# Kernel tuning notes

Measured on AMD Instinct MI355X. Metric: run time of the kernel, lower is better.

Reference implementation:

```python
import jax, jax.numpy as jnp
import numpy as np

HEADS = 8
DIM_HEAD = 64
SCALE = DIM_HEAD ** -0.5
EPS = 1e-5


def layernorm(t, g, b):
    mu = t.mean(-1, keepdims=True)
    var = ((t - mu) ** 2).mean(-1, keepdims=True)
    return (t - mu) * jax.lax.rsqrt(var + EPS) * g + b


def setup_inputs() -> dict:
    key = jax.random.key(0)
    ks = jax.random.split(key, 12)
    b, n, dim, inner = 2, 2048, 512, HEADS * DIM_HEAD
    s = dim ** -0.5
    return {
        "x": jax.random.normal(ks[0], (b, n, dim), jnp.float32),
        "context": jax.random.normal(ks[1], (b, n, dim), jnp.float32),
        "g_x": jnp.ones((dim,), jnp.float32),
        "b_x": jnp.zeros((dim,), jnp.float32),
        "g_c": jnp.ones((dim,), jnp.float32),
        "b_c": jnp.zeros((dim,), jnp.float32),
        "W_qk": jax.random.normal(ks[2], (dim, inner), jnp.float32) * s,
        "W_cqk": jax.random.normal(ks[3], (dim, inner), jnp.float32) * s,
        "W_v": jax.random.normal(ks[4], (dim, inner), jnp.float32) * s,
        "W_cv": jax.random.normal(ks[5], (dim, inner), jnp.float32) * s,
        "W_out": jax.random.normal(ks[6], (inner, dim), jnp.float32) * s,
        "b_out": jnp.zeros((dim,), jnp.float32),
        "W_cout": jax.random.normal(ks[7], (inner, dim), jnp.float32) * s,
        "b_cout": jnp.zeros((dim,), jnp.float32),
    }


def reference(x, context, g_x, b_x, g_c, b_c, W_qk, W_cqk, W_v, W_cv, W_out, b_out, W_cout, b_cout):
    b, i, _ = x.shape
    j = context.shape[1]
    xn = layernorm(x, g_x, b_x)
    cn = layernorm(context, g_c, b_c)

    def split_heads(t):  # [b, n, h*d] -> [b, h, n, d]
        return t.reshape(t.shape[0], t.shape[1], HEADS, DIM_HEAD).transpose(0, 2, 1, 3)

    qk = split_heads(xn @ W_qk)
    cqk = split_heads(cn @ W_cqk)
    v = split_heads(xn @ W_v)
    cv = split_heads(cn @ W_cv)

    sim = jnp.einsum('bhid,bhjd->bhij', qk, cqk) * SCALE  # [b,h,i,j]
    attn = jax.nn.softmax(sim, axis=-1)           # rows: x attends to context
    context_attn = jax.nn.softmax(sim, axis=-2)   # cols: context attends to x

    out = jnp.einsum('bhij,bhjd->bhid', attn, cv)            # [b,h,i,d]
    context_out = jnp.einsum('bhij,bhid->bhjd', context_attn, v)  # [b,h,j,d]

    def merge_heads(t):  # [b,h,n,d] -> [b,n,h*d]
        return t.transpose(0, 2, 1, 3).reshape(t.shape[0], t.shape[2], HEADS * DIM_HEAD)

    out = merge_heads(out) @ W_out + b_out
    context_out = merge_heads(context_out) @ W_cout + b_cout
    return out, context_out
```

## Files before the change

kernel.cpp:

```cpp
#include <hip/hip_runtime.h>


typedef _Float16 half_t;
typedef __attribute__((ext_vector_type(4))) _Float16 half4v;
typedef __attribute__((ext_vector_type(8))) _Float16 half8v;
typedef __attribute__((ext_vector_type(4))) float floatx4;

#define MFMA16(a, b, c) __builtin_amdgcn_mfma_f32_16x16x32_f16((a), (b), (c), 0, 0, 0)

#if defined(__has_builtin)
#if __has_builtin(__builtin_amdgcn_exp2f)
#define EXP2F(x) __builtin_amdgcn_exp2f(x)
#else
#define EXP2F(x) exp2f(x)
#endif
#else
#define EXP2F(x) exp2f(x)
#endif

__device__ __forceinline__ void gld16(const half_t* g, half_t* l) {
    __builtin_amdgcn_global_load_lds(
        (const __attribute__((address_space(1))) void*)g,
        (__attribute__((address_space(3))) void*)l, 16, 0, 0);
}

__global__ __launch_bounds__(256) void prep_kernel(
    const float* __restrict__ x, const float* __restrict__ ctx,
    const float* __restrict__ gx, const float* __restrict__ bx,
    const float* __restrict__ gc, const float* __restrict__ bc,
    half_t* __restrict__ xn, half_t* __restrict__ cn,
    const float* __restrict__ W0, const float* __restrict__ W1,
    const float* __restrict__ W2, const float* __restrict__ W3,
    const float* __restrict__ W4, const float* __restrict__ W5,
    half_t* __restrict__ Wt)
{
    __shared__ alignas(16) half_t Ts[128][136];
    const int blk = blockIdx.x;
    const int tid = threadIdx.x;
    const int wave = tid >> 6, lane = tid & 63;

    if (blk < 2048) {
        const int row = blk * 4 + wave;
        const float *src, *g, *b;
        half_t* dst;
        if (row < 4096) {
            src = x + (size_t)row * 512; g = gx; b = bx; dst = xn + (size_t)row * 512;
        } else {
            const size_t r = (size_t)(row - 4096);
            src = ctx + r * 512; g = gc; b = bc; dst = cn + r * 512;
        }
        const float4 a0 = *(const float4*)(src + lane * 4);
        const float4 a1 = *(const float4*)(src + 256 + lane * 4);
        float s = a0.x + a0.y + a0.z + a0.w + a1.x + a1.y + a1.z + a1.w;
        float q = a0.x * a0.x + a0.y * a0.y + a0.z * a0.z + a0.w * a0.w +
                  a1.x * a1.x + a1.y * a1.y + a1.z * a1.z + a1.w * a1.w;
#pragma unroll
        for (int m = 1; m < 64; m <<= 1) {
            s += __shfl_xor(s, m);
            q += __shfl_xor(q, m);
        }
        const float mean = s * (1.0f / 512.0f);
        const float var = q * (1.0f / 512.0f) - mean * mean;
        const float rs = rsqrtf(var + 1e-5f);
        const float4 g0 = *(const float4*)(g + lane * 4);
        const float4 g1 = *(const float4*)(g + 256 + lane * 4);
        const float4 b0 = *(const float4*)(b + lane * 4);
        const float4 b1 = *(const float4*)(b + 256 + lane * 4);
        half4v h0, h1;
        h0[0] = (half_t)((a0.x - mean) * rs * g0.x + b0.x);
        h0[1] = (half_t)((a0.y - mean) * rs * g0.y + b0.y);
        h0[2] = (half_t)((a0.z - mean) * rs * g0.z + b0.z);
        h0[3] = (half_t)((a0.w - mean) * rs * g0.w + b0.w);
        h1[0] = (half_t)((a1.x - mean) * rs * g1.x + b1.x);
        h1[1] = (half_t)((a1.y - mean) * rs * g1.y + b1.y);
        h1[2] = (half_t)((a1.z - mean) * rs * g1.z + b1.z);
        h1[3] = (half_t)((a1.w - mean) * rs * g1.w + b1.w);
        *(half4v*)(dst + lane * 4) = h0;
        *(half4v*)(dst + 256 + lane * 4) = h1;
        return;
    }

    const int b2 = blk - 2048;
    const int mat = b2 >> 4, tile = b2 & 15;
    const float* src;
    switch (mat) {
        case 0: src = W0; break;
        case 1: src = W1; break;
        case 2: src = W2; break;
        case 3: src = W3; break;
        case 4: src = W4; break;
        default: src = W5; break;
    }
    const int tr0 = (tile >> 2) * 128;
    const int tc0 = (tile & 3) * 128;
#pragma unroll
    for (int p = 0; p < 16; ++p) {
        const int idx = p * 256 + tid;
        const int r = idx >> 5, c4 = (idx & 31) * 4;
        const float4 w = *(const float4*)(src + (size_t)(tr0 + r) * 512 + tc0 + c4);
        Ts[c4 + 0][r] = (half_t)w.x;
        Ts[c4 + 1][r] = (half_t)w.y;
        Ts[c4 + 2][r] = (half_t)w.z;
        Ts[c4 + 3][r] = (half_t)w.w;
    }
    __syncthreads();
    half_t* dst = Wt + (size_t)mat * 262144;
#pragma unroll
    for (int p = 0; p < 8; ++p) {
        const int idx = p * 256 + tid;
        const int row = idx >> 4, ch = (idx & 15) * 8;
        *(half8v*)(dst + (size_t)(tc0 + row) * 512 + tr0 + ch) = *(const half8v*)&Ts[row][ch];
    }
}

__global__ __launch_bounds__(256) void gemm_in_kernel(
    const half_t* __restrict__ xn, const half_t* __restrict__ cn,
    const half_t* __restrict__ Wt,
    half_t* __restrict__ qk, half_t* __restrict__ v_t,
    half_t* __restrict__ cqk, half_t* __restrict__ cv_t)
{
    const half_t* A; const half_t* B; half_t* O;
    switch (blockIdx.z) {
        case 0:  A = xn; B = Wt;          O = qk;   break;
        case 1:  A = xn; B = Wt + 262144; O = v_t;  break;
        case 2:  A = cn; B = Wt + 524288; O = cqk;  break;
        default: A = cn; B = Wt + 786432; O = cv_t; break;
    }
    const int tr = blockIdx.z & 1;
    const int mt0 = blockIdx.x * 128;
    const int nt0 = blockIdx.y * 128;

    __shared__ alignas(16) half_t As[128 * 64];
    __shared__ alignas(16) half_t Ws[128 * 64];

    const int tid = threadIdx.x;
    const int wave = tid >> 6, lane = tid & 63;
    const int wr = wave >> 1, wc = wave & 1;
    const int q4 = lane >> 4, c = lane & 15;

    int srow[4], scol[4];
#pragma unroll
    for (int p = 0; p < 4; ++p) {
        const int ofs = p * 4096 + wave * 1024 + lane * 16;
        const int row = ofs >> 7;
        const int pc = (ofs >> 4) & 7;
        srow[p] = row;
        scol[p] = (pc ^ (row & 7)) * 8;
    }

    const half_t* P1 = tr ? As : Ws;
    const half_t* P2 = tr ? Ws : As;

    const floatx4 z4 = {0.f, 0.f, 0.f, 0.f};
    floatx4 acc[4][4];
#pragma unroll
    for (int mt = 0; mt < 4; ++mt)
#pragma unroll
        for (int nt = 0; nt < 4; ++nt) acc[mt][nt] = z4;

    for (int kb = 0; kb < 8; ++kb) {
        const int k0 = kb * 64;
#pragma unroll
        for (int p = 0; p < 4; ++p) {
            const int lofs = p * 2048 + wave * 512;
            gld16(A + (size_t)(mt0 + srow[p]) * 512 + k0 + scol[p], As + lofs);
            gld16(B + (size_t)(nt0 + srow[p]) * 512 + k0 + scol[p], Ws + lofs);
        }
        __syncthreads();
#pragma unroll
        for (int kt = 0; kt < 2; ++kt) {
            half8v f1[4], f2[4];
#pragma unroll
            for (int i = 0; i < 4; ++i) {
                const int r1 = wr * 64 + i * 16 + c;
                const int r2 = wc * 64 + i * 16 + c;
                f1[i] = *(const half8v*)&P1[(r1 << 6) + (((kt * 4 + q4) ^ (r1 & 7)) << 3)];
                f2[i] = *(const half8v*)&P2[(r2 << 6) + (((kt * 4 + q4) ^ (r2 & 7)) << 3)];
            }
#pragma unroll
            for (int mt = 0; mt < 4; ++mt)
#pragma unroll
                for (int nt = 0; nt < 4; ++nt)
                    acc[mt][nt] = MFMA16(f1[mt], f2[nt], acc[mt][nt]);
        }
        __syncthreads();
    }

    const int bb = mt0 >> 11;
    const int nnb = mt0 & 2047;
    if (tr) {
#pragma unroll
        for (int mt = 0; mt < 4; ++mt) {
            const int row = nnb + wr * 64 + mt * 16 + q4 * 4;
#pragma unroll
            for (int nt = 0; nt < 4; ++nt) {
                const int col = nt0 + wc * 64 + nt * 16 + c;
                const int h = col >> 6, dd = col & 63;
                half4v pk;
                pk[0] = (half_t)acc[mt][nt][0];
                pk[1] = (half_t)acc[mt][nt][1];
                pk[2] = (half_t)acc[mt][nt][2];
                pk[3] = (half_t)acc[mt][nt][3];
                *(half4v*)(O + ((size_t)(bb * 8 + h) * 64 + dd) * 2048 + row) = pk;
            }
        }
    } else {
#pragma unroll
        for (int mt = 0; mt < 4; ++mt) {
            const int colw = nt0 + wr * 64 + mt * 16 + q4 * 4;
            const int h = colw >> 6, dd = colw & 63;
#pragma unroll
            for (int nt = 0; nt < 4; ++nt) {
                const int row = nnb + wc * 64 + nt * 16 + c;
                half4v pk;
                pk[0] = (half_t)acc[mt][nt][0];
                pk[1] = (half_t)acc[mt][nt][1];
                pk[2] = (half_t)acc[mt][nt][2];
                pk[3] = (half_t)acc[mt][nt][3];
                *(half4v*)(O + ((size_t)(bb * 8 + h) * 2048 + row) * 64 + dd) = pk;
            }
        }
    }
}

__global__ __launch_bounds__(256, 2) void flash_kernel(
    const half_t* __restrict__ qk, const half_t* __restrict__ cqk,
    const half_t* __restrict__ v_t, const half_t* __restrict__ cv_t,
    half_t* __restrict__ out_h, half_t* __restrict__ ctx_out_h)
{
    const int it = blockIdx.x, bh = blockIdx.y, dir = blockIdx.z;
    const half_t* Q  = dir ? cqk : qk;
    const half_t* K  = dir ? qk  : cqk;
    const half_t* VT = dir ? v_t : cv_t;
    half_t* Out = dir ? ctx_out_h : out_h;
    const half_t* Qb = Q + (size_t)bh * (2048 * 64);
    const half_t* Kb = K + (size_t)bh * (2048 * 64);
    const half_t* VTb = VT + (size_t)bh * (64 * 2048);

    __shared__ alignas(16) half_t Ks[128][72];
    __shared__ alignas(16) half_t CVs[64][136];
    __shared__ alignas(16) half_t Ps[128][72];

    const int tid = threadIdx.x;
    const int wave = tid >> 6, lane = tid & 63;
    const int q4 = lane >> 4, c = lane & 15;

    half8v onesb;
#pragma unroll
    for (int j = 0; j < 8; ++j) onesb[j] = (c == 0) ? (half_t)1.0f : (half_t)0.0f;

    half8v qf[2][2];
#pragma unroll
    for (int mt = 0; mt < 2; ++mt)
#pragma unroll
        for (int kt = 0; kt < 2; ++kt) {
            half8v v = *(const half8v*)(Qb + (size_t)(it * 128 + wave * 32 + mt * 16 + c) * 64 +
                                        kt * 32 + q4 * 8);
            qf[mt][kt] = v * (half_t)0.18033688f;
        }

    const floatx4 z4 = {0.f, 0.f, 0.f, 0.f};
    floatx4 accT[4][2];
    floatx4 accL[2];
#pragma unroll
    for (int vt = 0; vt < 4; ++vt)
#pragma unroll
        for (int mt = 0; mt < 2; ++mt) accT[vt][mt] = z4;
    accL[0] = z4; accL[1] = z4;

    half8v kpre[4], vpre[4];
#pragma unroll
    for (int p = 0; p < 4; ++p) {
        const int cidx = p * 256 + tid;
        kpre[p] = *(const half8v*)(Kb + (size_t)(cidx >> 3) * 64 + (cidx & 7) * 8);
        vpre[p] = *(const half8v*)(VTb + (size_t)(cidx >> 4) * 2048 + (cidx & 15) * 8);
    }

    for (int jt = 0; jt < 16; ++jt) {
        __syncthreads();
#pragma unroll
        for (int p = 0; p < 4; ++p) {
            const int cidx = p * 256 + tid;
            *(half8v*)&Ks[cidx >> 3][(cidx & 7) * 8] = kpre[p];
            *(half8v*)&CVs[cidx >> 4][(cidx & 15) * 8] = vpre[p];
        }
        __syncthreads();
        if (jt < 15) {
            const half_t* Kt = Kb + (size_t)(jt + 1) * 8192;
            const half_t* Vt = VTb + (jt + 1) * 128;
#pragma unroll
            for (int p = 0; p < 4; ++p) {
                const int cidx = p * 256 + tid;
                kpre[p] = *(const half8v*)(Kt + (size_t)(cidx >> 3) * 64 + (cidx & 7) * 8);
                vpre[p] = *(const half8v*)(Vt + (size_t)(cidx >> 4) * 2048 + (cidx & 15) * 8);
            }
        }

        floatx4 s[2][8];
#pragma unroll
        for (int nt = 0; nt < 8; ++nt) {
            const half8v kf0 = *(const half8v*)&Ks[nt * 16 + c][q4 * 8];
            const half8v kf1 = *(const half8v*)&Ks[nt * 16 + c][32 + q4 * 8];
#pragma unroll
            for (int mt = 0; mt < 2; ++mt) {
                floatx4 t = MFMA16(qf[mt][0], kf0, z4);
                s[mt][nt] = MFMA16(qf[mt][1], kf1, t);
            }
        }

#pragma unroll
        for (int ch = 0; ch < 2; ++ch) {
#pragma unroll
            for (int mt = 0; mt < 2; ++mt)
#pragma unroll
                for (int nl = 0; nl < 4; ++nl) {
                    const int nt = ch * 4 + nl;
#pragma unroll
                    for (int r = 0; r < 4; ++r) {
                        const float e = EXP2F(fminf(s[mt][nt][r], 15.0f));
                        Ps[wave * 32 + mt * 16 + q4 * 4 + r][nl * 16 + c] = (half_t)e;
                    }
                }
#pragma unroll
            for (int ktl = 0; ktl < 2; ++ktl) {
                half8v pf[2];
#pragma unroll
                for (int mt = 0; mt < 2; ++mt)
                    pf[mt] = *(const half8v*)&Ps[wave * 32 + mt * 16 + c][ktl * 32 + q4 * 8];
#pragma unroll
                for (int vt = 0; vt < 4; ++vt) {
                    const half8v bf = *(const half8v*)&CVs[vt * 16 + c][(ch * 2 + ktl) * 32 + q4 * 8];
#pragma unroll
                    for (int mt = 0; mt < 2; ++mt)
                        accT[vt][mt] = MFMA16(bf, pf[mt], accT[vt][mt]);
                }
#pragma unroll
                for (int mt = 0; mt < 2; ++mt)
                    accL[mt] = MFMA16(onesb, pf[mt], accL[mt]);
            }
        }
    }

    const size_t ob = (size_t)(bh >> 3) * 2048 * 512 + (size_t)(bh & 7) * 64;
#pragma unroll
    for (int mt = 0; mt < 2; ++mt) {
        const float l = __shfl(accL[mt][0], c);
        const float rl = 1.0f / l;
        const int row = it * 128 + wave * 32 + mt * 16 + c;
#pragma unroll
        for (int vt = 0; vt < 4; ++vt) {
            half4v pk;
            pk[0] = (half_t)(accT[vt][mt][0] * rl);
            pk[1] = (half_t)(accT[vt][mt][1] * rl);
            pk[2] = (half_t)(accT[vt][mt][2] * rl);
            pk[3] = (half_t)(accT[vt][mt][3] * rl);
            *(half4v*)(Out + ob + (size_t)row * 512 + vt * 16 + q4 * 4) = pk;
        }
    }
}

__global__ __launch_bounds__(256) void gemm_out_kernel(
    const half_t* __restrict__ out_h, const half_t* __restrict__ ctx_out_h,
    const half_t* __restrict__ Wt,
    const float* __restrict__ bout, const float* __restrict__ bcout,
    float* __restrict__ dout)
{
    const half_t* A; const half_t* B; const float* bias; float* O;
    if (blockIdx.z == 0) { A = out_h;     B = Wt + 1048576; bias = bout;  O = dout; }
    else                 { A = ctx_out_h; B = Wt + 1310720; bias = bcout; O = dout + 2097152; }

    const int mt0 = blockIdx.x * 64;
    const int nt0 = blockIdx.y * 128;

    __shared__ alignas(16) half_t As[64 * 64];
    __shared__ alignas(16) half_t Ws[128 * 64];

    const int tid = threadIdx.x;
    const int wave = tid >> 6, lane = tid & 63;
    const int wr = wave >> 1, wc = wave & 1;
    const int q4 = lane >> 4, c = lane & 15;

    int srow[4], scol[4];
#pragma unroll
    for (int p = 0; p < 4; ++p) {
        const int ofs = p * 4096 + wave * 1024 + lane * 16;
        const int row = ofs >> 7;
        const int pc = (ofs >> 4) & 7;
        srow[p] = row;
        scol[p] = (pc ^ (row & 7)) * 8;
    }

    const floatx4 z4 = {0.f, 0.f, 0.f, 0.f};
    floatx4 acc[4][2];
#pragma unroll
    for (int mt = 0; mt < 4; ++mt)
#pragma unroll
        for (int nt = 0; nt < 2; ++nt) acc[mt][nt] = z4;

    for (int kb = 0; kb < 8; ++kb) {
        const int k0 = kb * 64;
#pragma unroll
        for (int p = 0; p < 4; ++p) {
            const int lofs = p * 2048 + wave * 512;
            gld16(B + (size_t)(nt0 + srow[p]) * 512 + k0 + scol[p], Ws + lofs);
            if (p < 2)
                gld16(A + (size_t)(mt0 + srow[p]) * 512 + k0 + scol[p], As + lofs);
        }
        __syncthreads();
#pragma unroll
        for (int kt = 0; kt < 2; ++kt) {
            half8v f1[4], f2[2];
#pragma unroll
            for (int i = 0; i < 4; ++i) {
                const int r1 = wr * 64 + i * 16 + c;
                f1[i] = *(const half8v*)&Ws[(r1 << 6) + (((kt * 4 + q4) ^ (r1 & 7)) << 3)];
            }
#pragma unroll
            for (int i = 0; i < 2; ++i) {
                const int r2 = wc * 32 + i * 16 + c;
                f2[i] = *(const half8v*)&As[(r2 << 6) + (((kt * 4 + q4) ^ (r2 & 7)) << 3)];
            }
#pragma unroll
            for (int mt = 0; mt < 4; ++mt)
#pragma unroll
                for (int nt = 0; nt < 2; ++nt)
                    acc[mt][nt] = MFMA16(f1[mt], f2[nt], acc[mt][nt]);
        }
        __syncthreads();
    }

#pragma unroll
    for (int mt = 0; mt < 4; ++mt) {
        const int col = nt0 + wr * 64 + mt * 16 + q4 * 4;
        const float4 bv = *(const float4*)(bias + col);
#pragma unroll
        for (int nt = 0; nt < 2; ++nt) {
            const int row = mt0 + wc * 32 + nt * 16 + c;
            float4 o;
            o.x = acc[mt][nt][0] + bv.x;
            o.y = acc[mt][nt][1] + bv.y;
            o.z = acc[mt][nt][2] + bv.z;
            o.w = acc[mt][nt][3] + bv.w;
            *(float4*)(O + (size_t)row * 512 + col) = o;
        }
    }
}

extern "C" void kernel_launch(void* const* d_in, const int* in_sizes, int n_in,
                              void* d_out, int out_size, void* d_ws, size_t ws_size,
                              hipStream_t stream)
{
    (void)in_sizes; (void)n_in; (void)out_size; (void)ws_size;
    const float* x      = (const float*)d_in[0];
    const float* ctx    = (const float*)d_in[1];
    const float* g_x    = (const float*)d_in[2];
    const float* b_x    = (const float*)d_in[3];
    const float* g_c    = (const float*)d_in[4];
    const float* b_c    = (const float*)d_in[5];
    const float* W_qk   = (const float*)d_in[6];
    const float* W_cqk  = (const float*)d_in[7];
    const float* W_v    = (const float*)d_in[8];
    const float* W_cv   = (const float*)d_in[9];
    const float* W_out  = (const float*)d_in[10];
    const float* b_out  = (const float*)d_in[11];
    const float* W_cout = (const float*)d_in[12];
    const float* b_cout = (const float*)d_in[13];
    float* out = (float*)d_out;

    half_t* ws = (half_t*)d_ws;
    const size_t SEG = 2097152;
    half_t* xn        = ws;
    half_t* cn        = ws + 1 * SEG;
    half_t* qk        = ws + 2 * SEG;
    half_t* cqk       = ws + 3 * SEG;
    half_t* v_t       = ws + 4 * SEG;
    half_t* cv_t      = ws + 5 * SEG;
    half_t* Wt        = ws + 6 * SEG;
    half_t* out_h     = xn;
    half_t* ctx_out_h = cn;

    prep_kernel<<<2144, 256, 0, stream>>>(x, ctx, g_x, b_x, g_c, b_c, xn, cn,
                                          W_qk, W_v, W_cqk, W_cv, W_out, W_cout, Wt);
    gemm_in_kernel<<<dim3(32, 4, 4), 256, 0, stream>>>(xn, cn, Wt, qk, v_t, cqk, cv_t);
    flash_kernel<<<dim3(16, 16, 2), 256, 0, stream>>>(qk, cqk, v_t, cv_t, out_h, ctx_out_h);
    gemm_out_kernel<<<dim3(64, 4, 2), 256, 0, stream>>>(out_h, ctx_out_h, Wt, b_out, b_cout, out);
}
```

Before: 180.3 us.

## Use two waves per flash block with 64 rows each and transposed score MFMA

```diff
diff --git a/kernel.cpp b/kernel.cpp
--- a/kernel.cpp
+++ b/kernel.cpp
@@ -223,12 +223,12 @@
     }
 }
 
-__global__ __launch_bounds__(256, 2) void flash_kernel(
+__global__ __launch_bounds__(128, 1) void flash_kernel(
     const half_t* __restrict__ qk, const half_t* __restrict__ cqk,
     const half_t* __restrict__ v_t, const half_t* __restrict__ cv_t,
     half_t* __restrict__ out_h, half_t* __restrict__ ctx_out_h)
 {
-    const int it = blockIdx.x, bh = blockIdx.y, dir = blockIdx.z;
+    const int bh = blockIdx.x, it = blockIdx.y, dir = blockIdx.z;
     const half_t* Q  = dir ? cqk : qk;
     const half_t* K  = dir ? qk  : cqk;
     const half_t* VT = dir ? v_t : cv_t;
@@ -244,34 +244,36 @@
     const int tid = threadIdx.x;
     const int wave = tid >> 6, lane = tid & 63;
     const int q4 = lane >> 4, c = lane & 15;
+    const int rbase = wave * 64;
 
     half8v onesb;
 #pragma unroll
     for (int j = 0; j < 8; ++j) onesb[j] = (c == 0) ? (half_t)1.0f : (half_t)0.0f;
 
-    half8v qf[2][2];
-#pragma unroll
-    for (int mt = 0; mt < 2; ++mt)
+    half8v qf[4][2];
+#pragma unroll
+    for (int mt = 0; mt < 4; ++mt)
 #pragma unroll
         for (int kt = 0; kt < 2; ++kt) {
-            half8v v = *(const half8v*)(Qb + (size_t)(it * 128 + wave * 32 + mt * 16 + c) * 64 +
+            half8v v = *(const half8v*)(Qb + (size_t)(it * 128 + rbase + mt * 16 + c) * 64 +
                                         kt * 32 + q4 * 8);
             qf[mt][kt] = v * (half_t)0.18033688f;
         }
 
     const floatx4 z4 = {0.f, 0.f, 0.f, 0.f};
-    floatx4 accT[4][2];
-    floatx4 accL[2];
+    floatx4 accT[4][4];
+    floatx4 accL[4];
 #pragma unroll
     for (int vt = 0; vt < 4; ++vt)
 #pragma unroll
-        for (int mt = 0; mt < 2; ++mt) accT[vt][mt] = z4;
-    accL[0] = z4; accL[1] = z4;
-
-    half8v kpre[4], vpre[4];
-#pragma unroll
-    for (int p = 0; p < 4; ++p) {
-        const int cidx = p * 256 + tid;
+        for (int mt = 0; mt < 4; ++mt) accT[vt][mt] = z4;
+#pragma unroll
+    for (int mt = 0; mt < 4; ++mt) accL[mt] = z4;
+
+    half8v kpre[8], vpre[8];
+#pragma unroll
+    for (int p = 0; p < 8; ++p) {
+        const int cidx = p * 128 + tid;
         kpre[p] = *(const half8v*)(Kb + (size_t)(cidx >> 3) * 64 + (cidx & 7) * 8);
         vpre[p] = *(const half8v*)(VTb + (size_t)(cidx >> 4) * 2048 + (cidx & 15) * 8);
     }
@@ -279,8 +281,8 @@
     for (int jt = 0; jt < 16; ++jt) {
         __syncthreads();
 #pragma unroll
-        for (int p = 0; p < 4; ++p) {
-            const int cidx = p * 256 + tid;
+        for (int p = 0; p < 8; ++p) {
+            const int cidx = p * 128 + tid;
             *(half8v*)&Ks[cidx >> 3][(cidx & 7) * 8] = kpre[p];
             *(half8v*)&CVs[cidx >> 4][(cidx & 15) * 8] = vpre[p];
         }
@@ -289,53 +291,53 @@
             const half_t* Kt = Kb + (size_t)(jt + 1) * 8192;
             const half_t* Vt = VTb + (jt + 1) * 128;
 #pragma unroll
-            for (int p = 0; p < 4; ++p) {
-                const int cidx = p * 256 + tid;
+            for (int p = 0; p < 8; ++p) {
+                const int cidx = p * 128 + tid;
                 kpre[p] = *(const half8v*)(Kt + (size_t)(cidx >> 3) * 64 + (cidx & 7) * 8);
                 vpre[p] = *(const half8v*)(Vt + (size_t)(cidx >> 4) * 2048 + (cidx & 15) * 8);
             }
         }
 
-        floatx4 s[2][8];
-#pragma unroll
-        for (int nt = 0; nt < 8; ++nt) {
-            const half8v kf0 = *(const half8v*)&Ks[nt * 16 + c][q4 * 8];
-            const half8v kf1 = *(const half8v*)&Ks[nt * 16 + c][32 + q4 * 8];
-#pragma unroll
-            for (int mt = 0; mt < 2; ++mt) {
-                floatx4 t = MFMA16(qf[mt][0], kf0, z4);
-                s[mt][nt] = MFMA16(qf[mt][1], kf1, t);
-            }
-        }
-
 #pragma unroll
         for (int ch = 0; ch < 2; ++ch) {
-#pragma unroll
-            for (int mt = 0; mt < 2; ++mt)
+            floatx4 st[4][4];
+#pragma unroll
+            for (int nl = 0; nl < 4; ++nl) {
+                const int nt = ch * 4 + nl;
+                const half8v kf0 = *(const half8v*)&Ks[nt * 16 + c][q4 * 8];
+                const half8v kf1 = *(const half8v*)&Ks[nt * 16 + c][32 + q4 * 8];
+#pragma unroll
+                for (int mt = 0; mt < 4; ++mt) {
+                    floatx4 t = MFMA16(kf0, qf[mt][0], z4);
+                    st[mt][nl] = MFMA16(kf1, qf[mt][1], t);
+                }
+            }
+#pragma unroll
+            for (int mt = 0; mt < 4; ++mt)
 #pragma unroll
                 for (int nl = 0; nl < 4; ++nl) {
-                    const int nt = ch * 4 + nl;
-#pragma unroll
-                    for (int r = 0; r < 4; ++r) {
-                        const float e = EXP2F(fminf(s[mt][nt][r], 15.0f));
-                        Ps[wave * 32 + mt * 16 + q4 * 4 + r][nl * 16 + c] = (half_t)e;
-                    }
+                    half4v pk;
+#pragma unroll
+                    for (int r = 0; r < 4; ++r)
+                        pk[r] = (half_t)EXP2F(fminf(st[mt][nl][r], 15.0f));
+                    *(half4v*)&Ps[rbase + mt * 16 + c][(ch * 4 + nl) * 16 + q4 * 4] = pk;
                 }
 #pragma unroll
             for (int ktl = 0; ktl < 2; ++ktl) {
-                half8v pf[2];
-#pragma unroll
-                for (int mt = 0; mt < 2; ++mt)
-                    pf[mt] = *(const half8v*)&Ps[wave * 32 + mt * 16 + c][ktl * 32 + q4 * 8];
+                const int kofs = ch * 64 + ktl * 32 + q4 * 8;
+                half8v pf[4];
+#pragma unroll
+                for (int mt = 0; mt < 4; ++mt)
+                    pf[mt] = *(const half8v*)&Ps[rbase + mt * 16 + c][kofs];
 #pragma unroll
                 for (int vt = 0; vt < 4; ++vt) {
-                    const half8v bf = *(const half8v*)&CVs[vt * 16 + c][(ch * 2 + ktl) * 32 + q4 * 8];
-#pragma unroll
-                    for (int mt = 0; mt < 2; ++mt)
+                    const half8v bf = *(const half8v*)&CVs[vt * 16 + c][kofs];
+#pragma unroll
+                    for (int mt = 0; mt < 4; ++mt)
                         accT[vt][mt] = MFMA16(bf, pf[mt], accT[vt][mt]);
                 }
 #pragma unroll
-                for (int mt = 0; mt < 2; ++mt)
+                for (int mt = 0; mt < 4; ++mt)
                     accL[mt] = MFMA16(onesb, pf[mt], accL[mt]);
             }
         }
@@ -343,10 +345,10 @@
 
     const size_t ob = (size_t)(bh >> 3) * 2048 * 512 + (size_t)(bh & 7) * 64;
 #pragma unroll
-    for (int mt = 0; mt < 2; ++mt) {
+    for (int mt = 0; mt < 4; ++mt) {
         const float l = __shfl(accL[mt][0], c);
         const float rl = 1.0f / l;
-        const int row = it * 128 + wave * 32 + mt * 16 + c;
+        const int row = it * 128 + rbase + mt * 16 + c;
 #pragma unroll
         for (int vt = 0; vt < 4; ++vt) {
             half4v pk;
@@ -482,6 +484,6 @@
     prep_kernel<<<2144, 256, 0, stream>>>(x, ctx, g_x, b_x, g_c, b_c, xn, cn,
                                           W_qk, W_v, W_cqk, W_cv, W_out, W_cout, Wt);
     gemm_in_kernel<<<dim3(32, 4, 4), 256, 0, stream>>>(xn, cn, Wt, qk, v_t, cqk, cv_t);
-    flash_kernel<<<dim3(16, 16, 2), 256, 0, stream>>>(qk, cqk, v_t, cv_t, out_h, ctx_out_h);
+    flash_kernel<<<dim3(16, 16, 2), 128, 0, stream>>>(qk, cqk, v_t, cv_t, out_h, ctx_out_h);
     gemm_out_kernel<<<dim3(64, 4, 2), 256, 0, stream>>>(out_h, ctx_out_h, Wt, b_out, b_cout, out);
 }
```

Result: slower. 194.4 us (+7.8%).

## Keep softmax probabilities in registers and swizzle K/V shared-memory layout

Applied to the files above, without the earlier changes.

```diff
diff --git a/kernel.cpp b/kernel.cpp
--- a/kernel.cpp
+++ b/kernel.cpp
@@ -2,6 +2,7 @@
 
 
 typedef _Float16 half_t;
+typedef __attribute__((ext_vector_type(2))) _Float16 half2v;
 typedef __attribute__((ext_vector_type(4))) _Float16 half4v;
 typedef __attribute__((ext_vector_type(8))) _Float16 half8v;
 typedef __attribute__((ext_vector_type(4))) float floatx4;
@@ -17,6 +18,16 @@
 #else
 #define EXP2F(x) exp2f(x)
 #endif
+
+__device__ __forceinline__ half2v pk2(float a, float b) {
+#if defined(__has_builtin) && __has_builtin(__builtin_amdgcn_cvt_pkrtz)
+    union { __fp16 __attribute__((ext_vector_type(2))) i; half2v o; } u;
+    u.i = __builtin_amdgcn_cvt_pkrtz(a, b);
+    return u.o;
+#else
+    half2v r; r[0] = (half_t)a; r[1] = (half_t)b; return r;
+#endif
+}
 
 __device__ __forceinline__ void gld16(const half_t* g, half_t* l) {
     __builtin_amdgcn_global_load_lds(
@@ -228,7 +239,7 @@
     const half_t* __restrict__ v_t, const half_t* __restrict__ cv_t,
     half_t* __restrict__ out_h, half_t* __restrict__ ctx_out_h)
 {
-    const int it = blockIdx.x, bh = blockIdx.y, dir = blockIdx.z;
+    const int bh = blockIdx.x, it = blockIdx.y, dir = blockIdx.z;
     const half_t* Q  = dir ? cqk : qk;
     const half_t* K  = dir ? qk  : cqk;
     const half_t* VT = dir ? v_t : cv_t;
@@ -237,9 +248,8 @@
     const half_t* Kb = K + (size_t)bh * (2048 * 64);
     const half_t* VTb = VT + (size_t)bh * (64 * 2048);
 
-    __shared__ alignas(16) half_t Ks[128][72];
-    __shared__ alignas(16) half_t CVs[64][136];
-    __shared__ alignas(16) half_t Ps[128][72];
+    __shared__ alignas(16) half_t Ks[128 * 64];
+    __shared__ alignas(16) half_t CVs[64 * 128];
 
     const int tid = threadIdx.x;
     const int wave = tid >> 6, lane = tid & 63;
@@ -281,8 +291,10 @@
 #pragma unroll
         for (int p = 0; p < 4; ++p) {
             const int cidx = p * 256 + tid;
-            *(half8v*)&Ks[cidx >> 3][(cidx & 7) * 8] = kpre[p];
-            *(half8v*)&CVs[cidx >> 4][(cidx & 15) * 8] = vpre[p];
+            const int krow = cidx >> 3, kch = cidx & 7;
+            *(half8v*)&Ks[krow * 64 + ((kch ^ ((krow >> 2) & 7)) * 8)] = kpre[p];
+            const int vrow = cidx >> 4, vch = cidx & 15;
+            *(half8v*)&CVs[vrow * 128 + ((vch ^ (vrow & 15)) * 8)] = vpre[p];
         }
         __syncthreads();
         if (jt < 15) {
@@ -296,48 +308,46 @@
             }
         }
 
-        floatx4 s[2][8];
-#pragma unroll
-        for (int nt = 0; nt < 8; ++nt) {
-            const half8v kf0 = *(const half8v*)&Ks[nt * 16 + c][q4 * 8];
-            const half8v kf1 = *(const half8v*)&Ks[nt * 16 + c][32 + q4 * 8];
+#pragma unroll
+        for (int g = 0; g < 4; ++g) {
+            floatx4 st[2][2];
+#pragma unroll
+            for (int t = 0; t < 2; ++t) {
+                const int jr = g * 32 + t * 4 + ((c >> 2) << 3) + (c & 3);
+                const int sw = (jr >> 2) & 7;
+                const half8v kf0 = *(const half8v*)&Ks[jr * 64 + ((q4 ^ sw) * 8)];
+                const half8v kf1 = *(const half8v*)&Ks[jr * 64 + (((4 + q4) ^ sw) * 8)];
+#pragma unroll
+                for (int mt = 0; mt < 2; ++mt) {
+                    floatx4 tt = MFMA16(kf0, qf[mt][0], z4);
+                    st[mt][t] = MFMA16(kf1, qf[mt][1], tt);
+                }
+            }
+            half8v pf[2];
 #pragma unroll
             for (int mt = 0; mt < 2; ++mt) {
-                floatx4 t = MFMA16(qf[mt][0], kf0, z4);
-                s[mt][nt] = MFMA16(qf[mt][1], kf1, t);
-            }
-        }
-
-#pragma unroll
-        for (int ch = 0; ch < 2; ++ch) {
+                union { half8v v; half2v h2[4]; } u;
+                u.h2[0] = pk2(EXP2F(fminf(st[mt][0][0], 15.0f)),
+                              EXP2F(fminf(st[mt][0][1], 15.0f)));
+                u.h2[1] = pk2(EXP2F(fminf(st[mt][0][2], 15.0f)),
+                              EXP2F(fminf(st[mt][0][3], 15.0f)));
+                u.h2[2] = pk2(EXP2F(fminf(st[mt][1][0], 15.0f)),
+                              EXP2F(fminf(st[mt][1][1], 15.0f)));
+                u.h2[3] = pk2(EXP2F(fminf(st[mt][1][2], 15.0f)),
+                              EXP2F(fminf(st[mt][1][3], 15.0f)));
+                pf[mt] = u.v;
+            }
+#pragma unroll
+            for (int vt = 0; vt < 4; ++vt) {
+                const half8v bf = *(const half8v*)&CVs[(vt * 16 + c) * 128 +
+                                                       (((g * 4 + q4) ^ c) * 8)];
+#pragma unroll
+                for (int mt = 0; mt < 2; ++mt)
+                    accT[vt][mt] = MFMA16(bf, pf[mt], accT[vt][mt]);
+            }
 #pragma unroll
             for (int mt = 0; mt < 2; ++mt)
-#pragma unroll
-                for (int nl = 0; nl < 4; ++nl) {
-                    const int nt = ch * 4 + nl;
-#pragma unroll
-                    for (int r = 0; r < 4; ++r) {
-                        const float e = EXP2F(fminf(s[mt][nt][r], 15.0f));
-                        Ps[wave * 32 + mt * 16 + q4 * 4 + r][nl * 16 + c] = (half_t)e;
-                    }
-                }
-#pragma unroll
-            for (int ktl = 0; ktl < 2; ++ktl) {
-                half8v pf[2];
-#pragma unroll
-                for (int mt = 0; mt < 2; ++mt)
-                    pf[mt] = *(const half8v*)&Ps[wave * 32 + mt * 16 + c][ktl * 32 + q4 * 8];
-#pragma unroll
-                for (int vt = 0; vt < 4; ++vt) {
-                    const half8v bf = *(const half8v*)&CVs[vt * 16 + c][(ch * 2 + ktl) * 32 + q4 * 8];
-#pragma unroll
-                    for (int mt = 0; mt < 2; ++mt)
-                        accT[vt][mt] = MFMA16(bf, pf[mt], accT[vt][mt]);
-                }
-#pragma unroll
-                for (int mt = 0; mt < 2; ++mt)
-                    accL[mt] = MFMA16(onesb, pf[mt], accL[mt]);
-            }
+                accL[mt] = MFMA16(onesb, pf[mt], accL[mt]);
         }
     }
 
```

After: 171.7 us. 1.05x faster.
